# Kernel tuning notes

Measured on AMD Instinct MI355X. Metric: run time of the kernel, lower is better.

The kernel has to match this reference:

```python
import jax, jax.numpy as jnp
import numpy as np

B, N, D = 8, 256, 128


def setup_inputs() -> dict:
    key = jax.random.key(0)
    ks = jax.random.split(key, 4)
    s1 = 1.0 / np.sqrt(4 * D)
    s2 = 1.0 / np.sqrt(2 * D)
    s3 = 1.0 / np.sqrt(D)
    return {
        "tour_features": jax.random.normal(ks[0], (B, N, D), dtype=jnp.float32),
        "W1": jax.random.uniform(ks[1], (4 * D, 2 * D), jnp.float32, -s1, s1),
        "b1": jnp.zeros((2 * D,), jnp.float32),
        "W2": jax.random.uniform(ks[2], (2 * D, D), jnp.float32, -s2, s2),
        "b2": jnp.zeros((D,), jnp.float32),
        "W3": jax.random.uniform(ks[3], (D, 1), jnp.float32, -s3, s3),
        "b3": jnp.zeros((1,), jnp.float32),
    }


def reference(tour_features, W1, b1, W2, b2, W3, b3):
    Bs, Ns, Ds = tour_features.shape
    x = tour_features
    x_next = jnp.roll(x, -1, axis=1)  # node at (k+1) % N
    # Split first linear's weight by the 4 concatenated feature blocks:
    # cat([x_i, x_{i+1}, x_j, x_{j+1}]) @ W1 == x_i@W1a + x_{i+1}@W1b + x_j@W1c + x_{j+1}@W1d
    W1a, W1b, W1c, W1d = jnp.split(W1, 4, axis=0)
    Pi = x @ W1a + x_next @ W1b          # [B, N, 2D] (i-side projection)
    Pj = x @ W1c + x_next @ W1d          # [B, N, 2D] (j-side projection)
    h1 = jax.nn.relu(Pi[:, :, None, :] + Pj[:, None, :, :] + b1)  # [B, N, N, 2D]
    h2 = jax.nn.relu(h1 @ W2 + b2)       # [B, N, N, D]
    score = jnp.tanh((h2 @ W3 + b3)[..., 0])  # [B, N, N]
    # Valid pairs: j >= i + 2 and not (j - i == N - 1)
    ii = jnp.arange(Ns)[:, None]
    jj = jnp.arange(Ns)[None, :]
    mask = (jj >= ii + 2) & (jj - ii != Ns - 1)
    improvement_matrix = jnp.where(mask[None], score, 0.0)
    improved_tour = jnp.broadcast_to(jnp.arange(Ns), (Bs, Ns))
    return improved_tour, improvement_matrix
```

## Files before the change

kernel.cpp:

```cpp
#include <hip/hip_runtime.h>


typedef __attribute__((ext_vector_type(8))) short short8;
typedef __attribute__((ext_vector_type(8))) _Float16 half8;
typedef __attribute__((ext_vector_type(4))) float floatx4;

static __device__ __forceinline__ unsigned short f2bf(float f) {
  unsigned int x = __float_as_uint(f);
  x += 0x7fff + ((x >> 16) & 1);
  return (unsigned short)(x >> 16);
}

static __device__ __forceinline__ unsigned short f2h(float f) {
  _Float16 h = (_Float16)f;
  return __builtin_bit_cast(unsigned short, h);
}

static __device__ __forceinline__ float fast_tanh(float x) {
  float e = __expf(2.0f * fabsf(x));
  float t = 1.0f - 2.0f * __builtin_amdgcn_rcpf(e + 1.0f);
  return copysignf(t, x);
}

static __device__ __forceinline__ long pack_fp8(half8 s) {
  int lo = __builtin_amdgcn_cvt_pk_fp8_f32((float)s[0], (float)s[1], 0, false);
  lo = __builtin_amdgcn_cvt_pk_fp8_f32((float)s[2], (float)s[3], lo, true);
  int hi = __builtin_amdgcn_cvt_pk_fp8_f32((float)s[4], (float)s[5], 0, false);
  hi = __builtin_amdgcn_cvt_pk_fp8_f32((float)s[6], (float)s[7], hi, true);
  return (long)(unsigned)lo | ((long)hi << 32);
}

static __device__ __forceinline__ void gload_lds16(const void* g, void* l) {
  __builtin_amdgcn_global_load_lds(
      (const __attribute__((address_space(1))) unsigned int*)g,
      (__attribute__((address_space(3))) unsigned int*)l, 16, 0, 0);
}

__global__ __launch_bounds__(256) void k_prep(
    const float* __restrict__ x, const float* __restrict__ W1,
    const float* __restrict__ W2, float* __restrict__ out,
    unsigned char* __restrict__ W2F8, unsigned short* __restrict__ W1T,
    unsigned short* __restrict__ xcat) {
  int e = blockIdx.x * 256 + threadIdx.x;
  if (e < 2048) {
    out[e] = (float)(e & 255);
  } else if (e < 526336) {
    out[e] = 0.f;
  } else if (e < 542720) {
    int t = e - 526336;
    int p = t >> 7, n = t & 127;
    float f0 = W2[(2 * p) * 128 + n] * 16.f;
    float f1 = W2[(2 * p + 1) * 128 + n] * 16.f;
    int v2 = __builtin_amdgcn_cvt_pk_fp8_f32(f0, f1, 0, false);
    int col = 2 * p;
    int sw = (((col >> 4) ^ (n & 15)) << 4) | (col & 15);
    *(unsigned short*)(W2F8 + n * 256 + sw) = (unsigned short)(v2 & 0xffff);
  } else if (e < 673792) {
    int e3 = e - 542720;
    int n = e3 >> 8, k = e3 & 255;
    int v = k >> 3;
    int sw = (((v & 16) | ((v ^ (n & 15)) & 15)) << 3) | (k & 7);
    W1T[(n << 8) + sw] = f2bf(W1[((k + (n & 256)) << 8) + (n & 255)]);
  } else {
    int e4 = e - 673792;
    int r = e4 >> 8, k = e4 & 255;
    int v = k >> 3;
    int sw = (((v & 16) | ((v ^ (r & 15)) & 15)) << 3) | (k & 7);
    int pos = r & 255;
    int pos2 = (k < 128) ? pos : ((pos + 1) & 255);
    xcat[(r << 8) + sw] = f2bf(x[(((r >> 8) << 8) + pos2) * 128 + (k & 127)]);
  }
}

__global__ __launch_bounds__(256) void k_proj(
    const unsigned short* __restrict__ xcat, const unsigned short* __restrict__ W1T,
    const float* __restrict__ b1, unsigned short* __restrict__ PiH,
    unsigned short* __restrict__ PjH) {
  const int mg = blockIdx.x >> 3;
  const int ng = blockIdx.x & 7;
  const int tid = threadIdx.x;
  const int wr = tid >> 6, lane = tid & 63, quad = lane >> 4, l15 = lane & 15;

  __shared__ unsigned short As[64 * 256];
  __shared__ unsigned short Bs[64 * 256];

  const unsigned short* Asrc = xcat + mg * 64 * 256;
  const unsigned short* Bsrc = W1T + ng * 64 * 256;
#pragma unroll
  for (int it = 0; it < 8; ++it) {
    const int c = it * 256 + wr * 64 + lane;
    gload_lds16(Asrc + c * 8, &As[(it * 256 + wr * 64) * 8]);
    gload_lds16(Bsrc + c * 8, &Bs[(it * 256 + wr * 64) * 8]);
  }
  __syncthreads();

  floatx4 acc[4];
#pragma unroll
  for (int mt = 0; mt < 4; ++mt) acc[mt] = (floatx4)0.f;

  const char* Ab = (const char*)As;
  const char* Bb = (const char*)Bs + wr * 16 * 512;
  const int base_sw = l15 * 512 + ((quad ^ l15) << 4);

#pragma unroll
  for (int ks = 0; ks < 8; ++ks) {
    const int swz = base_sw ^ (ks << 6);
    short8 bfr = *(const short8*)(Bb + swz);
#pragma unroll
    for (int mt = 0; mt < 4; ++mt) {
      short8 afr = *(const short8*)(Ab + mt * 8192 + swz);
      acc[mt] = __builtin_amdgcn_mfma_f32_16x16x32_bf16(afr, bfr, acc[mt], 0, 0, 0);
    }
  }

  const int ch = ng * 64 + wr * 16 + l15;
  const float bias = (ch < 256) ? b1[ch] : 0.f;
  unsigned short* dst = (ch < 256) ? PiH : PjH;
  const int chan = ch & 255;
#pragma unroll
  for (int mt = 0; mt < 4; ++mt)
#pragma unroll
    for (int r = 0; r < 4; ++r) {
      int row = mg * 64 + mt * 16 + quad * 4 + r;
      dst[row * 256 + chan] = f2h(acc[mt][r] + bias);
    }
}

__global__ __launch_bounds__(256, 3) void k_main(
    const unsigned short* __restrict__ PiH, const unsigned short* __restrict__ PjH,
    const unsigned char* __restrict__ W2F8, const float* __restrict__ b2,
    const float* __restrict__ W3, const float* __restrict__ b3,
    float* __restrict__ outm) {
  const int tid = threadIdx.x;
  const int wr = tid >> 6;
  const int lane = tid & 63, quad = lane >> 4, l15 = lane & 15;

  __shared__ unsigned char W2s[128 * 256];

#pragma unroll
  for (int it = 0; it < 8; ++it) {
    const int c = it * 256 + wr * 64 + lane;
    gload_lds16(W2F8 + c * 16, &W2s[(it * 256 + wr * 64) * 16]);
  }
  __syncthreads();

  const int e2 = blockIdx.x * 4 + wr;
  const int b = (int)(((unsigned)e2 * 14769u) >> 24);
  const int e = e2 - b * 1136;
  int jt = 0, base = 0;
  if (e >= 30)  { jt = 1; base = 30;  }
  if (e >= 92)  { jt = 2; base = 92;  }
  if (e >= 186) { jt = 3; base = 186; }
  if (e >= 312) { jt = 4; base = 312; }
  if (e >= 470) { jt = 5; base = 470; }
  if (e >= 660) { jt = 6; base = 660; }
  if (e >= 882) { jt = 7; base = 882; }
  const int i = e - base;

  const char* W2base = (const char*)&W2s[0];
  const int base_sw = l15 * 256 + ((((quad >> 1) ^ l15) & 15) << 4) + ((quad & 1) << 3);
  const unsigned short* Pjb = PjH + ((b << 8) + jt * 32 + l15) * 256 + quad * 8;
  const unsigned short* PiRow = PiH + ((b << 8) + i) * 256 + quad * 8;

  floatx4 acc[2][8];
#pragma unroll
  for (int mt = 0; mt < 2; ++mt)
#pragma unroll
    for (int nt = 0; nt < 8; ++nt) acc[mt][nt] = (floatx4)0.f;

  union U4 { uint4 v; half8 h; };
  U4 piR[2], pjR[2][2];
  piR[0].v = *(const uint4*)(PiRow);
  pjR[0][0].v = *(const uint4*)(Pjb);
  pjR[0][1].v = *(const uint4*)(Pjb + 4096);

  long bfrA[8], bfrB[8];
  {
    const char* b0 = W2base + base_sw;
#pragma unroll
    for (int nt = 0; nt < 8; ++nt) bfrA[nt] = *(const long*)(b0 + nt * 4096);
  }

#pragma unroll
  for (int ks = 0; ks < 8; ++ks) {
    const int cur = ks & 1, nxt = cur ^ 1;
    if (ks < 7) {
      const char* bn = W2base + (base_sw ^ ((ks + 1) << 5));
#pragma unroll
      for (int nt = 0; nt < 8; ++nt)
        ((ks & 1) ? bfrA : bfrB)[nt] = *(const long*)(bn + nt * 4096);
    }
    if (ks < 7) {
      piR[nxt].v = *(const uint4*)(PiRow + (ks + 1) * 32);
      pjR[nxt][0].v = *(const uint4*)(Pjb + (ks + 1) * 32);
      pjR[nxt][1].v = *(const uint4*)(Pjb + 4096 + (ks + 1) * 32);
    }
    const half8 s0 = __builtin_elementwise_max(piR[cur].h + pjR[cur][0].h,
                                               (half8)(_Float16)0);
    const half8 s1 = __builtin_elementwise_max(piR[cur].h + pjR[cur][1].h,
                                               (half8)(_Float16)0);
    const long a0 = pack_fp8(s0);
    const long a1 = pack_fp8(s1);
    const long* bc = (ks & 1) ? bfrB : bfrA;
    __builtin_amdgcn_s_setprio(1);
#pragma unroll
    for (int nt = 0; nt < 8; ++nt) {
      acc[0][nt] = __builtin_amdgcn_mfma_f32_16x16x32_fp8_fp8(a0, bc[nt], acc[0][nt], 0, 0, 0);
      acc[1][nt] = __builtin_amdgcn_mfma_f32_16x16x32_fp8_fp8(a1, bc[nt], acc[1][nt], 0, 0, 0);
    }
    __builtin_amdgcn_s_setprio(0);
  }

  float* orow = outm + ((b << 8) + i) * 256 + jt * 32;
  const float b3v = b3[0];
  const float s16 = 0.0625f;
#pragma unroll
  for (int mt = 0; mt < 2; ++mt) {
    float p0 = 0, p1 = 0, p2 = 0, p3 = 0;
#pragma unroll
    for (int nt = 0; nt < 8; ++nt) {
      float w3v = W3[nt * 16 + l15];
      float b2v = b2[nt * 16 + l15];
      floatx4 a = acc[mt][nt];
      p0 += fmaxf(fmaf(a[0], s16, b2v), 0.f) * w3v;
      p1 += fmaxf(fmaf(a[1], s16, b2v), 0.f) * w3v;
      p2 += fmaxf(fmaf(a[2], s16, b2v), 0.f) * w3v;
      p3 += fmaxf(fmaf(a[3], s16, b2v), 0.f) * w3v;
    }
#pragma unroll
    for (int m = 8; m >= 1; m >>= 1) {
      p0 += __shfl_xor(p0, m, 16);
      p1 += __shfl_xor(p1, m, 16);
      p2 += __shfl_xor(p2, m, 16);
      p3 += __shfl_xor(p3, m, 16);
    }
    if (l15 == 0) {
      const int jl = jt * 32 + mt * 16 + quad * 4;
      float ps[4] = {p0, p1, p2, p3};
#pragma unroll
      for (int r = 0; r < 4; ++r) {
        int j = jl + r;
        float sc = fast_tanh(ps[r] + b3v);
        bool valid = (j >= i + 2) && (j - i != 255);
        orow[mt * 16 + quad * 4 + r] = valid ? sc : 0.f;
      }
    }
  }
}

extern "C" void kernel_launch(void* const* d_in, const int* in_sizes, int n_in,
                              void* d_out, int out_size, void* d_ws, size_t ws_size,
                              hipStream_t stream) {
  const float* x  = (const float*)d_in[0];
  const float* W1 = (const float*)d_in[1];
  const float* b1 = (const float*)d_in[2];
  const float* W2 = (const float*)d_in[3];
  const float* b2 = (const float*)d_in[4];
  const float* W3 = (const float*)d_in[5];
  const float* b3 = (const float*)d_in[6];
  float* out = (float*)d_out;

  unsigned short* PiH  = (unsigned short*)d_ws;
  unsigned short* PjH  = PiH + 524288;
  unsigned short* W1T  = PjH + 524288;
  unsigned short* xcat = W1T + 131072;
  unsigned char*  W2F8 = (unsigned char*)(xcat + 524288);

  k_prep<<<4680, 256, 0, stream>>>(x, W1, W2, out, W2F8, W1T, xcat);
  k_proj<<<256, 256, 0, stream>>>(xcat, W1T, b1, PiH, PjH);
  k_main<<<2272, 256, 0, stream>>>(PiH, PjH, W2F8, b2, W3, b3, out + 2048);
}
```

Before: 101.5 us.

## Stage Pi/Pj tiles in LDS and widen W2 fragment reads to 16 bytes

```diff
diff --git a/kernel.cpp b/kernel.cpp
--- a/kernel.cpp
+++ b/kernel.cpp
@@ -52,9 +52,11 @@
     float f0 = W2[(2 * p) * 128 + n] * 16.f;
     float f1 = W2[(2 * p + 1) * 128 + n] * 16.f;
     int v2 = __builtin_amdgcn_cvt_pk_fp8_f32(f0, f1, 0, false);
-    int col = 2 * p;
-    int sw = (((col >> 4) ^ (n & 15)) << 4) | (col & 15);
-    *(unsigned short*)(W2F8 + n * 256 + sw) = (unsigned short)(v2 & 0xffff);
+    int q = n >> 5, which = (n >> 4) & 1, l = n & 15;
+    int c = p >> 2, off = (p & 3) * 2;
+    int cs = (c & 16) | ((c ^ l) & 15);
+    *(unsigned short*)(W2F8 + q * 8192 + l * 512 + cs * 16 + which * 8 + off) =
+        (unsigned short)(v2 & 0xffff);
   } else if (e < 673792) {
     int e3 = e - 542720;
     int n = e3 >> 8, k = e3 & 255;
@@ -115,14 +117,22 @@
 
   const int ch = ng * 64 + wr * 16 + l15;
   const float bias = (ch < 256) ? b1[ch] : 0.f;
-  unsigned short* dst = (ch < 256) ? PiH : PjH;
+  const bool isPi = (ch < 256);
+  unsigned short* dst = isPi ? PiH : PjH;
   const int chan = ch & 255;
+  const int ck = chan >> 3, coff = chan & 7;
 #pragma unroll
   for (int mt = 0; mt < 4; ++mt)
 #pragma unroll
     for (int r = 0; r < 4; ++r) {
       int row = mg * 64 + mt * 16 + quad * 4 + r;
-      dst[row * 256 + chan] = f2h(acc[mt][r] + bias);
+      int cpos;
+      if (isPi) cpos = chan;
+      else {
+        int cs = (ck & 16) | ((ck ^ (row & 15)) & 15);
+        cpos = cs * 8 + coff;
+      }
+      dst[row * 256 + cpos] = f2h(acc[mt][r] + bias);
     }
 }
 
@@ -135,32 +145,44 @@
   const int wr = tid >> 6;
   const int lane = tid & 63, quad = lane >> 4, l15 = lane & 15;
 
-  __shared__ unsigned char W2s[128 * 256];
-
+  __shared__ unsigned char W2s[32768];
+  __shared__ unsigned char PjS[16384];
+  __shared__ unsigned char PiS[4096];
+
+  const int bid = blockIdx.x;
+  const int b = bid / 288;
+  const int rem = bid - b * 288;
+  int jt = 0, basej = 0;
+  if (rem >= 8)   { jt = 1; basej = 8;   }
+  if (rem >= 24)  { jt = 2; basej = 24;  }
+  if (rem >= 48)  { jt = 3; basej = 48;  }
+  if (rem >= 80)  { jt = 4; basej = 80;  }
+  if (rem >= 120) { jt = 5; basej = 120; }
+  if (rem >= 168) { jt = 6; basej = 168; }
+  if (rem >= 224) { jt = 7; basej = 224; }
+  const int i = (rem - basej) * 4 + wr;
+
+  const unsigned char* pjsrc =
+      (const unsigned char*)(PjH + ((b << 8) + jt * 32) * 256);
+  const unsigned char* pisrc =
+      (const unsigned char*)(PiH + ((b << 8) + i) * 256);
 #pragma unroll
   for (int it = 0; it < 8; ++it) {
     const int c = it * 256 + wr * 64 + lane;
     gload_lds16(W2F8 + c * 16, &W2s[(it * 256 + wr * 64) * 16]);
   }
+#pragma unroll
+  for (int it = 0; it < 4; ++it) {
+    const int c = it * 256 + wr * 64 + lane;
+    gload_lds16(pjsrc + c * 16, &PjS[(it * 256 + wr * 64) * 16]);
+  }
+  gload_lds16(pisrc + (lane & 31) * 16, &PiS[wr * 1024]);
   __syncthreads();
 
-  const int e2 = blockIdx.x * 4 + wr;
-  const int b = (int)(((unsigned)e2 * 14769u) >> 24);
-  const int e = e2 - b * 1136;
-  int jt = 0, base = 0;
-  if (e >= 30)  { jt = 1; base = 30;  }
-  if (e >= 92)  { jt = 2; base = 92;  }
-  if (e >= 186) { jt = 3; base = 186; }
-  if (e >= 312) { jt = 4; base = 312; }
-  if (e >= 470) { jt = 5; base = 470; }
-  if (e >= 660) { jt = 6; base = 660; }
-  if (e >= 882) { jt = 7; base = 882; }
-  const int i = e - base;
-
   const char* W2base = (const char*)&W2s[0];
-  const int base_sw = l15 * 256 + ((((quad >> 1) ^ l15) & 15) << 4) + ((quad & 1) << 3);
-  const unsigned short* Pjb = PjH + ((b << 8) + jt * 32 + l15) * 256 + quad * 8;
-  const unsigned short* PiRow = PiH + ((b << 8) + i) * 256 + quad * 8;
+  const char* PjBase = (const char*)&PjS[0];
+  const char* PiBase = (const char*)&PiS[0] + wr * 1024 + quad * 16;
+  const int sw16 = l15 * 512 + (((quad ^ l15) & 15) << 4);
 
   floatx4 acc[2][8];
 #pragma unroll
@@ -170,30 +192,31 @@
 
   union U4 { uint4 v; half8 h; };
   U4 piR[2], pjR[2][2];
-  piR[0].v = *(const uint4*)(PiRow);
-  pjR[0][0].v = *(const uint4*)(Pjb);
-  pjR[0][1].v = *(const uint4*)(Pjb + 4096);
-
-  long bfrA[8], bfrB[8];
+  piR[0].v = *(const uint4*)(PiBase);
+  pjR[0][0].v = *(const uint4*)(PjBase + sw16);
+  pjR[0][1].v = *(const uint4*)(PjBase + 8192 + sw16);
+
+  uint4 bfA[4], bfB[4];
   {
-    const char* b0 = W2base + base_sw;
-#pragma unroll
-    for (int nt = 0; nt < 8; ++nt) bfrA[nt] = *(const long*)(b0 + nt * 4096);
+    const char* b0 = W2base + sw16;
+#pragma unroll
+    for (int q = 0; q < 4; ++q) bfA[q] = *(const uint4*)(b0 + q * 8192);
   }
 
 #pragma unroll
   for (int ks = 0; ks < 8; ++ks) {
     const int cur = ks & 1, nxt = cur ^ 1;
     if (ks < 7) {
-      const char* bn = W2base + (base_sw ^ ((ks + 1) << 5));
-#pragma unroll
-      for (int nt = 0; nt < 8; ++nt)
-        ((ks & 1) ? bfrA : bfrB)[nt] = *(const long*)(bn + nt * 4096);
+      const char* bn = W2base + (sw16 ^ ((ks + 1) << 6));
+#pragma unroll
+      for (int q = 0; q < 4; ++q)
+        ((ks & 1) ? bfA : bfB)[q] = *(const uint4*)(bn + q * 8192);
     }
     if (ks < 7) {
-      piR[nxt].v = *(const uint4*)(PiRow + (ks + 1) * 32);
-      pjR[nxt][0].v = *(const uint4*)(Pjb + (ks + 1) * 32);
-      pjR[nxt][1].v = *(const uint4*)(Pjb + 4096 + (ks + 1) * 32);
+      piR[nxt].v = *(const uint4*)(PiBase + (ks + 1) * 64);
+      const char* pj = PjBase + (sw16 ^ ((ks + 1) << 6));
+      pjR[nxt][0].v = *(const uint4*)(pj);
+      pjR[nxt][1].v = *(const uint4*)(pj + 8192);
     }
     const half8 s0 = __builtin_elementwise_max(piR[cur].h + pjR[cur][0].h,
                                                (half8)(_Float16)0);
@@ -201,12 +224,16 @@
                                                (half8)(_Float16)0);
     const long a0 = pack_fp8(s0);
     const long a1 = pack_fp8(s1);
-    const long* bc = (ks & 1) ? bfrB : bfrA;
+    const uint4* bc = (ks & 1) ? bfB : bfA;
     __builtin_amdgcn_s_setprio(1);
 #pragma unroll
-    for (int nt = 0; nt < 8; ++nt) {
-      acc[0][nt] = __builtin_amdgcn_mfma_f32_16x16x32_fp8_fp8(a0, bc[nt], acc[0][nt], 0, 0, 0);
-      acc[1][nt] = __builtin_amdgcn_mfma_f32_16x16x32_fp8_fp8(a1, bc[nt], acc[1][nt], 0, 0, 0);
+    for (int q = 0; q < 4; ++q) {
+      const long blo = (long)bc[q].x | ((long)bc[q].y << 32);
+      const long bhi = (long)bc[q].z | ((long)bc[q].w << 32);
+      acc[0][2 * q]     = __builtin_amdgcn_mfma_f32_16x16x32_fp8_fp8(a0, blo, acc[0][2 * q], 0, 0, 0);
+      acc[1][2 * q]     = __builtin_amdgcn_mfma_f32_16x16x32_fp8_fp8(a1, blo, acc[1][2 * q], 0, 0, 0);
+      acc[0][2 * q + 1] = __builtin_amdgcn_mfma_f32_16x16x32_fp8_fp8(a0, bhi, acc[0][2 * q + 1], 0, 0, 0);
+      acc[1][2 * q + 1] = __builtin_amdgcn_mfma_f32_16x16x32_fp8_fp8(a1, bhi, acc[1][2 * q + 1], 0, 0, 0);
     }
     __builtin_amdgcn_s_setprio(0);
   }
@@ -268,5 +295,5 @@
 
   k_prep<<<4680, 256, 0, stream>>>(x, W1, W2, out, W2F8, W1T, xcat);
   k_proj<<<256, 256, 0, stream>>>(xcat, W1T, b1, PiH, PjH);
-  k_main<<<2272, 256, 0, stream>>>(PiH, PjH, W2F8, b2, W3, b3, out + 2048);
-}
+  k_main<<<2304, 256, 0, stream>>>(PiH, PjH, W2F8, b2, W3, b3, out + 2048);
+}
```

Measured after the change: 96.96 us. 1.05x faster.
